# Kernel tuning notes

Measured on AMD Instinct MI355X. Metric: run time of the kernel, lower is better.

The kernel has to match this reference:

```python
import jax, jax.numpy as jnp
import numpy as np
from jax import lax

DN = ('NCDHW', 'OIDHW', 'NCDHW')


def _ln(x, w, b, eps=1e-5):
    m = jnp.mean(x, -1, keepdims=True)
    v = jnp.mean((x - m) ** 2, -1, keepdims=True)
    return (x - m) * lax.rsqrt(v + eps) * w + b


def _gelu(x):
    return jax.nn.gelu(x, approximate=False)


def _dwconv3(v, w, b, groups):
    # depthwise 3x3x3, padding=1, stride=1; v:[B,C,H,W,D], w:[C,1,3,3,3]
    y = lax.conv_general_dilated(v, w, (1, 1, 1), 'SAME',
                                 dimension_numbers=DN,
                                 feature_group_count=groups)
    return y + b[None, :, None, None, None]


def _forward(x, ln1_w, ln1_b, q_w, sr1_w, sr1_b, n1_w, n1_b, sr2_w, sr2_b,
             n2_w, n2_b, kv1_w, kv2_w, lc1_w, lc1_b, lc2_w, lc2_b,
             proj_w, proj_b, ln2_w, ln2_b, fc1_w, fc1_b, fc2_w, fc2_b,
             H, W, D):
    B, N, C = x.shape
    h = 8
    h2 = h // 2
    hd = C // h
    scale = hd ** -0.5
    C2 = C // 2

    # ---- pre-norm + attention ----
    xa = _ln(x, ln1_w, ln1_b)
    q = (xa @ q_w.T).reshape(B, N, h, hd).transpose(0, 2, 1, 3)  # [B,h,N,hd]

    x_ = xa.transpose(0, 2, 1).reshape(B, C, H, W, D)
    # branch 1: conv k=2 s=2 spatial reduction
    y1 = lax.conv_general_dilated(x_, sr1_w, (2, 2, 2), 'VALID',
                                  dimension_numbers=DN) + sr1_b[None, :, None, None, None]
    N1 = (H // 2) * (W // 2) * (D // 2)
    x1 = _gelu(_ln(y1.reshape(B, C, N1).transpose(0, 2, 1), n1_w, n1_b))  # [B,N1,C]
    # branch 2: 1x1x1 conv, full resolution
    y2 = lax.conv_general_dilated(x_, sr2_w, (1, 1, 1), 'VALID',
                                  dimension_numbers=DN) + sr2_b[None, :, None, None, None]
    N2 = N
    x2 = _gelu(_ln(y2.reshape(B, C, N2).transpose(0, 2, 1), n2_w, n2_b))  # [B,N2,C]

    kv1 = (x1 @ kv1_w.T).reshape(B, N1, 2, h2, hd).transpose(2, 0, 3, 1, 4)
    k1, v1 = kv1[0], kv1[1]  # [B,h2,N1,hd]
    kv2 = (x2 @ kv2_w.T).reshape(B, N2, 2, h2, hd).transpose(2, 0, 3, 1, 4)
    k2, v2 = kv2[0], kv2[1]  # [B,h2,N2,hd]

    attn1 = jax.nn.softmax(jnp.einsum('bhnd,bhmd->bhnm', q[:, :h2], k1) * scale, axis=-1)
    v1sp = v1.transpose(0, 2, 1, 3).reshape(B, N1, C2).transpose(0, 2, 1).reshape(
        B, C2, H // 2, W // 2, D // 2)
    v1 = v1 + _dwconv3(v1sp, lc1_w, lc1_b, C2).reshape(B, h2, hd, N1).transpose(0, 1, 3, 2)
    o1 = jnp.einsum('bhnm,bhmd->bhnd', attn1, v1).transpose(0, 2, 1, 3).reshape(B, N, C2)

    attn2 = jax.nn.softmax(jnp.einsum('bhnd,bhmd->bhnm', q[:, h2:], k2) * scale, axis=-1)
    v2sp = v2.transpose(0, 2, 1, 3).reshape(B, N2, C2).transpose(0, 2, 1).reshape(B, C2, H, W, D)
    v2 = v2 + _dwconv3(v2sp, lc2_w, lc2_b, C2).reshape(B, h2, hd, N2).transpose(0, 1, 3, 2)
    o2 = jnp.einsum('bhnm,bhmd->bhnd', attn2, v2).transpose(0, 2, 1, 3).reshape(B, N, C2)

    att = jnp.concatenate([o1, o2], axis=-1) @ proj_w.T + proj_b
    x = x + att  # residual (drop_path = 0)

    # ---- pre-norm + MLP ----
    xm = _ln(x, ln2_w, ln2_b)
    mlp = _gelu(xm @ fc1_w.T + fc1_b) @ fc2_w.T + fc2_b
    return x + mlp


def setup_inputs() -> dict:
    key = jax.random.key(0)
    B, C, H, W, D = 2, 384, 16, 16, 16
    N = H * W * D
    hid = 4 * C
    C2 = C // 2
    ks = iter(jax.random.split(key, 32))
    rn = lambda shape, s=0.02: (jax.random.normal(next(ks), shape) * s).astype(jnp.float32)
    return {
        'x': jax.random.normal(next(ks), (B, N, C), jnp.float32),
        'ln1_w': jnp.ones(C, jnp.float32), 'ln1_b': jnp.zeros(C, jnp.float32),
        'q_w': rn((C, C)),
        'sr1_w': rn((C, C, 2, 2, 2), 0.025), 'sr1_b': jnp.zeros(C, jnp.float32),
        'n1_w': jnp.ones(C, jnp.float32), 'n1_b': jnp.zeros(C, jnp.float32),
        'sr2_w': rn((C, C, 1, 1, 1), 0.07), 'sr2_b': jnp.zeros(C, jnp.float32),
        'n2_w': jnp.ones(C, jnp.float32), 'n2_b': jnp.zeros(C, jnp.float32),
        'kv1_w': rn((C, C)), 'kv2_w': rn((C, C)),
        'lc1_w': rn((C2, 1, 3, 3, 3), 0.27), 'lc1_b': jnp.zeros(C2, jnp.float32),
        'lc2_w': rn((C2, 1, 3, 3, 3), 0.27), 'lc2_b': jnp.zeros(C2, jnp.float32),
        'proj_w': rn((C, C)), 'proj_b': jnp.zeros(C, jnp.float32),
        'ln2_w': jnp.ones(C, jnp.float32), 'ln2_b': jnp.zeros(C, jnp.float32),
        'fc1_w': rn((hid, C)), 'fc1_b': jnp.zeros(hid, jnp.float32),
        'fc2_w': rn((C, hid)), 'fc2_b': jnp.zeros(C, jnp.float32),
        'H': H, 'W': W, 'D': D,
    }


def reference(x, ln1_w, ln1_b, q_w, sr1_w, sr1_b, n1_w, n1_b, sr2_w, sr2_b,
              n2_w, n2_b, kv1_w, kv2_w, lc1_w, lc1_b, lc2_w, lc2_b,
              proj_w, proj_b, ln2_w, ln2_b, fc1_w, fc1_b, fc2_w, fc2_b,
              H, W, D):
    return _forward(x, ln1_w, ln1_b, q_w, sr1_w, sr1_b, n1_w, n1_b, sr2_w, sr2_b,
                    n2_w, n2_b, kv1_w, kv2_w, lc1_w, lc1_b, lc2_w, lc2_b,
                    proj_w, proj_b, ln2_w, ln2_b, fc1_w, fc1_b, fc2_w, fc2_b,
                    H, W, D)
```

## Files before the change

kernel.cpp:

```cpp
#include <hip/hip_runtime.h>

typedef unsigned short ushort_t;
typedef unsigned int uint_t;
typedef __bf16 bf16_t;
typedef __bf16 bf16x8 __attribute__((ext_vector_type(8)));
typedef float f32x4 __attribute__((ext_vector_type(4)));

__device__ __forceinline__ float b2f(ushort_t u) {
    union { uint_t i; float f; } v; v.i = ((uint_t)u) << 16; return v.f;
}
__device__ __forceinline__ ushort_t f2b(float f) {
    union { float f; uint_t i; } v; v.f = f;
    uint_t r = v.i + 0x7fffu + ((v.i >> 16) & 1u);
    return (ushort_t)(r >> 16);
}
__device__ __forceinline__ float gelu_exact(float x) {
    return 0.5f * x * (1.0f + erff(x * 0.70710678118654752f));
}

__global__ void prep_weights(const float* __restrict__ q_w, const float* __restrict__ sr2_w,
                             const float* __restrict__ kv1_w, const float* __restrict__ kv2_w,
                             const float* __restrict__ proj_w, const float* __restrict__ fc1_w,
                             const float* __restrict__ fc2_w, const float* __restrict__ sr1_w,
                             ushort_t* __restrict__ dst) {
    int gid = blockIdx.x * 256 + threadIdx.x;
    int i = gid;
    if (i < 147456) { dst[gid] = f2b(q_w[i]); return; }
    i -= 147456;
    if (i < 147456) { dst[gid] = f2b(sr2_w[i]); return; }
    i -= 147456;
    if (i < 147456) { dst[gid] = f2b(kv1_w[i]); return; }
    i -= 147456;
    if (i < 147456) { dst[gid] = f2b(kv2_w[i]); return; }
    i -= 147456;
    if (i < 147456) { dst[gid] = f2b(proj_w[i]); return; }
    i -= 147456;
    if (i < 589824) { dst[gid] = f2b(fc1_w[i]); return; }
    i -= 589824;
    if (i < 589824) { dst[gid] = f2b(fc2_w[i]); return; }
    i -= 589824;
    if (i < 1179648) {
        int co = i / 3072, r = i % 3072, kk = r / 384, ci = r % 384;
        dst[gid] = f2b(sr1_w[((size_t)co * 384 + ci) * 8 + kk]);
    }
}

__global__ void im2col_kernel(const ushort_t* __restrict__ xa, ushort_t* __restrict__ A1) {
    int gid = blockIdx.x * 256 + threadIdx.x;
    if (gid >= 1024 * 3072) return;
    int m = gid / 3072, r = gid % 3072, kk = r / 384, ci = r % 384;
    int b = m >> 9, n1 = m & 511;
    int ho = n1 >> 6, wo = (n1 >> 3) & 7, dz = n1 & 7;
    int n = ((2 * ho + ((kk >> 2) & 1)) << 8) + ((2 * wo + ((kk >> 1) & 1)) << 4) + (2 * dz + (kk & 1));
    A1[gid] = xa[((size_t)b * 4096 + n) * 384 + ci];
}

__global__ __launch_bounds__(128) void ln_kernel(const float* __restrict__ in,
                                                 const float* __restrict__ w,
                                                 const float* __restrict__ b,
                                                 float* __restrict__ outf,
                                                 ushort_t* __restrict__ outb, int act) {
    const int C = 384;
    int row = blockIdx.x, tid = threadIdx.x;
    size_t base = (size_t)row * C;
    float x[3], s = 0.f, s2 = 0.f;
#pragma unroll
    for (int i = 0; i < 3; i++) {
        int c = tid + i * 128;
        float v = in[base + c];
        x[i] = v; s += v; s2 += v * v;
    }
    for (int off = 32; off; off >>= 1) { s += __shfl_down(s, off); s2 += __shfl_down(s2, off); }
    __shared__ float sc[4];
    int lane = tid & 63, wid = tid >> 6;
    if (lane == 0) { sc[wid] = s; sc[wid + 2] = s2; }
    __syncthreads();
    float ts = sc[0] + sc[1], ts2 = sc[2] + sc[3];
    float mean = ts / C;
    float var = ts2 / C - mean * mean;
    float rstd = rsqrtf(var + 1e-5f);
#pragma unroll
    for (int i = 0; i < 3; i++) {
        int c = tid + i * 128;
        float v = (x[i] - mean) * rstd * w[c] + b[c];
        if (act) v = gelu_exact(v);
        if (outf) outf[base + c] = v;
        if (outb) outb[base + c] = f2b(v);
    }
}

__global__ __launch_bounds__(256) void mfma_gemm(const ushort_t* __restrict__ A,
                                                 const ushort_t* __restrict__ W,
                                                 const float* __restrict__ bias,
                                                 const float* __restrict__ res,
                                                 float* __restrict__ outf,
                                                 ushort_t* __restrict__ outb,
                                                 int M, int N, int K, int act) {
    __shared__ bf16_t Asl[128][40];
    __shared__ bf16_t Wsl[128][40];
    int tid = threadIdx.x;
    int wave = tid >> 6, lane = tid & 63, g = lane >> 4, c = lane & 15;
    int wm = wave >> 1, wn = wave & 1;
    int m0 = blockIdx.y * 128, n0 = blockIdx.x * 128;
    int srow = tid >> 1, sseg = tid & 1;
    const ushort_t* Abase = A + (size_t)(m0 + srow) * K + sseg * 16;
    const ushort_t* Wbase = W + (size_t)(n0 + srow) * K + sseg * 16;

    f32x4 acc[4][4];
#pragma unroll
    for (int i = 0; i < 4; i++)
#pragma unroll
        for (int j = 0; j < 4; j++) acc[i][j] = f32x4{0.f, 0.f, 0.f, 0.f};

    uint4 av0 = *(const uint4*)Abase, av1 = *(const uint4*)(Abase + 8);
    uint4 wv0 = *(const uint4*)Wbase, wv1 = *(const uint4*)(Wbase + 8);
    for (int k0 = 0; k0 < K; k0 += 32) {
        __syncthreads();
        *(uint4*)&Asl[srow][sseg * 16] = av0;
        *(uint4*)&Asl[srow][sseg * 16 + 8] = av1;
        *(uint4*)&Wsl[srow][sseg * 16] = wv0;
        *(uint4*)&Wsl[srow][sseg * 16 + 8] = wv1;
        __syncthreads();
        uint4 nav0, nav1, nwv0, nwv1;
        bool more = (k0 + 32 < K);
        if (more) {
            nav0 = *(const uint4*)(Abase + k0 + 32);
            nav1 = *(const uint4*)(Abase + k0 + 40);
            nwv0 = *(const uint4*)(Wbase + k0 + 32);
            nwv1 = *(const uint4*)(Wbase + k0 + 40);
        }
        bf16x8 af[4], bf[4];
#pragma unroll
        for (int fi = 0; fi < 4; fi++) af[fi] = *(bf16x8*)&Asl[wm * 64 + fi * 16 + c][g * 8];
#pragma unroll
        for (int fj = 0; fj < 4; fj++) bf[fj] = *(bf16x8*)&Wsl[wn * 64 + fj * 16 + c][g * 8];
#pragma unroll
        for (int fi = 0; fi < 4; fi++)
#pragma unroll
            for (int fj = 0; fj < 4; fj++)
                acc[fi][fj] = __builtin_amdgcn_mfma_f32_16x16x32_bf16(af[fi], bf[fj], acc[fi][fj], 0, 0, 0);
        if (more) { av0 = nav0; av1 = nav1; wv0 = nwv0; wv1 = nwv1; }
    }

#pragma unroll
    for (int fi = 0; fi < 4; fi++) {
#pragma unroll
        for (int fj = 0; fj < 4; fj++) {
            int n = n0 + wn * 64 + fj * 16 + c;
            float bv = bias ? bias[n] : 0.f;
#pragma unroll
            for (int i = 0; i < 4; i++) {
                int m = m0 + wm * 64 + fi * 16 + 4 * g + i;
                float v = acc[fi][fj][i] + bv;
                if (act == 1) v = gelu_exact(v);
                size_t idx = (size_t)m * N + n;
                if (res) v += res[idx];
                if (outf) outf[idx] = v;
                if (outb) outb[idx] = f2b(v);
            }
        }
    }
}

__global__ __launch_bounds__(256) void gemm64(const ushort_t* __restrict__ A,
                                              const ushort_t* __restrict__ W,
                                              const float* __restrict__ bias,
                                              const float* __restrict__ res,
                                              float* __restrict__ outf,
                                              ushort_t* __restrict__ outb,
                                              int M, int N, int K, int act, float oscale) {
    __shared__ bf16_t Asl[64][72];
    __shared__ bf16_t Wsl[64][72];
    int tid = threadIdx.x;
    int wave = tid >> 6, lane = tid & 63, g = lane >> 4, c = lane & 15;
    int wm = wave >> 1, wn = wave & 1;
    int m0 = blockIdx.y * 64, n0 = blockIdx.x * 64;
    int srow = tid >> 2, sseg = tid & 3;
    const ushort_t* Abase = A + (size_t)(m0 + srow) * K + sseg * 16;
    const ushort_t* Wbase = W + (size_t)(n0 + srow) * K + sseg * 16;

    f32x4 acc[2][2];
#pragma unroll
    for (int i = 0; i < 2; i++)
#pragma unroll
        for (int j = 0; j < 2; j++) acc[i][j] = f32x4{0.f, 0.f, 0.f, 0.f};

    uint4 av0 = *(const uint4*)Abase, av1 = *(const uint4*)(Abase + 8);
    uint4 wv0 = *(const uint4*)Wbase, wv1 = *(const uint4*)(Wbase + 8);
    for (int k0 = 0; k0 < K; k0 += 64) {
        __syncthreads();
        *(uint4*)&Asl[srow][sseg * 16] = av0;
        *(uint4*)&Asl[srow][sseg * 16 + 8] = av1;
        *(uint4*)&Wsl[srow][sseg * 16] = wv0;
        *(uint4*)&Wsl[srow][sseg * 16 + 8] = wv1;
        __syncthreads();
        uint4 nav0, nav1, nwv0, nwv1;
        bool more = (k0 + 64 < K);
        if (more) {
            nav0 = *(const uint4*)(Abase + k0 + 64);
            nav1 = *(const uint4*)(Abase + k0 + 72);
            nwv0 = *(const uint4*)(Wbase + k0 + 64);
            nwv1 = *(const uint4*)(Wbase + k0 + 72);
        }
#pragma unroll
        for (int kk = 0; kk < 2; kk++) {
            bf16x8 af[2], bf[2];
#pragma unroll
            for (int fi = 0; fi < 2; fi++) af[fi] = *(bf16x8*)&Asl[wm * 32 + fi * 16 + c][kk * 32 + g * 8];
#pragma unroll
            for (int fj = 0; fj < 2; fj++) bf[fj] = *(bf16x8*)&Wsl[wn * 32 + fj * 16 + c][kk * 32 + g * 8];
#pragma unroll
            for (int fi = 0; fi < 2; fi++)
#pragma unroll
                for (int fj = 0; fj < 2; fj++)
                    acc[fi][fj] = __builtin_amdgcn_mfma_f32_16x16x32_bf16(af[fi], bf[fj], acc[fi][fj], 0, 0, 0);
        }
        if (more) { av0 = nav0; av1 = nav1; wv0 = nwv0; wv1 = nwv1; }
    }

#pragma unroll
    for (int fi = 0; fi < 2; fi++) {
#pragma unroll
        for (int fj = 0; fj < 2; fj++) {
            int n = n0 + wn * 32 + fj * 16 + c;
            float bv = bias ? bias[n] : 0.f;
#pragma unroll
            for (int i = 0; i < 4; i++) {
                int m = m0 + wm * 32 + fi * 16 + 4 * g + i;
                float v = (acc[fi][fj][i] + bv) * oscale;
                if (act == 1) v = gelu_exact(v);
                size_t idx = (size_t)m * N + n;
                if (res) v += res[idx];
                if (outf) outf[idx] = v;
                if (outb) outb[idx] = f2b(v);
            }
        }
    }
}

__global__ __launch_bounds__(256) void gemm_qy2(const ushort_t* __restrict__ A,
                                                const ushort_t* __restrict__ W,
                                                const float* __restrict__ sr2_b,
                                                ushort_t* __restrict__ qb,
                                                float* __restrict__ y2f,
                                                int M, float qscale) {
    const int K = 384;
    __shared__ bf16_t Asl[64][72];
    __shared__ bf16_t Wsl[64][72];
    int tid = threadIdx.x;
    int wave = tid >> 6, lane = tid & 63, g = lane >> 4, c = lane & 15;
    int wm = wave >> 1, wn = wave & 1;
    int m0 = blockIdx.y * 64, n0 = blockIdx.x * 64;
    int srow = tid >> 2, sseg = tid & 3;
    const ushort_t* Abase = A + (size_t)(m0 + srow) * K + sseg * 16;
    const ushort_t* Wbase = W + (size_t)(n0 + srow) * K + sseg * 16;

    f32x4 acc[2][2];
#pragma unroll
    for (int i = 0; i < 2; i++)
#pragma unroll
        for (int j = 0; j < 2; j++) acc[i][j] = f32x4{0.f, 0.f, 0.f, 0.f};

    uint4 av0 = *(const uint4*)Abase, av1 = *(const uint4*)(Abase + 8);
    uint4 wv0 = *(const uint4*)Wbase, wv1 = *(const uint4*)(Wbase + 8);
    for (int k0 = 0; k0 < K; k0 += 64) {
        __syncthreads();
        *(uint4*)&Asl[srow][sseg * 16] = av0;
        *(uint4*)&Asl[srow][sseg * 16 + 8] = av1;
        *(uint4*)&Wsl[srow][sseg * 16] = wv0;
        *(uint4*)&Wsl[srow][sseg * 16 + 8] = wv1;
        __syncthreads();
        uint4 nav0, nav1, nwv0, nwv1;
        bool more = (k0 + 64 < K);
        if (more) {
            nav0 = *(const uint4*)(Abase + k0 + 64);
            nav1 = *(const uint4*)(Abase + k0 + 72);
            nwv0 = *(const uint4*)(Wbase + k0 + 64);
            nwv1 = *(const uint4*)(Wbase + k0 + 72);
        }
#pragma unroll
        for (int kk = 0; kk < 2; kk++) {
            bf16x8 af[2], bf[2];
#pragma unroll
            for (int fi = 0; fi < 2; fi++) af[fi] = *(bf16x8*)&Asl[wm * 32 + fi * 16 + c][kk * 32 + g * 8];
#pragma unroll
            for (int fj = 0; fj < 2; fj++) bf[fj] = *(bf16x8*)&Wsl[wn * 32 + fj * 16 + c][kk * 32 + g * 8];
#pragma unroll
            for (int fi = 0; fi < 2; fi++)
#pragma unroll
                for (int fj = 0; fj < 2; fj++)
                    acc[fi][fj] = __builtin_amdgcn_mfma_f32_16x16x32_bf16(af[fi], bf[fj], acc[fi][fj], 0, 0, 0);
        }
        if (more) { av0 = nav0; av1 = nav1; wv0 = nwv0; wv1 = nwv1; }
    }

    int isq = (n0 < 384);
#pragma unroll
    for (int fi = 0; fi < 2; fi++) {
#pragma unroll
        for (int fj = 0; fj < 2; fj++) {
            int n = n0 + wn * 32 + fj * 16 + c;
#pragma unroll
            for (int i = 0; i < 4; i++) {
                int m = m0 + wm * 32 + fi * 16 + 4 * g + i;
                float v = acc[fi][fj][i];
                if (isq) {
                    qb[(size_t)m * 384 + n] = f2b(v * qscale);
                } else {
                    y2f[(size_t)m * 384 + (n - 384)] = v + sr2_b[n - 384];
                }
            }
        }
    }
}

__device__ __forceinline__ void dwconv_one(const ushort_t* __restrict__ vin,
                                           const float* __restrict__ wt,
                                           const float* __restrict__ bias,
                                           ushort_t* __restrict__ vout,
                                           int Hs, int Wsz, int Ds, int S, int gid) {
    int c2 = gid % 192;
    int r = gid / 192;
    int n = r % S;
    int b = r / S;
    int dz = n % Ds, wy = (n / Ds) % Wsz, hx = n / (Wsz * Ds);
    float center = b2f(vin[(size_t)(b * S + n) * 384 + c2]);
    float acc = bias[c2];
    for (int kh = -1; kh <= 1; kh++) {
        int h2 = hx + kh; if (h2 < 0 || h2 >= Hs) continue;
        for (int kw = -1; kw <= 1; kw++) {
            int w2 = wy + kw; if (w2 < 0 || w2 >= Wsz) continue;
            for (int kd = -1; kd <= 1; kd++) {
                int d2 = dz + kd; if (d2 < 0 || d2 >= Ds) continue;
                int nn = (h2 * Wsz + w2) * Ds + d2;
                acc += b2f(vin[(size_t)(b * S + nn) * 384 + c2]) *
                       wt[c2 * 27 + (kh + 1) * 9 + (kw + 1) * 3 + (kd + 1)];
            }
        }
    }
    vout[(size_t)(b * S + n) * 192 + c2] = f2b(center + acc);
}

__global__ void dwconv2_kernel(const ushort_t* __restrict__ v2in, const ushort_t* __restrict__ v1in,
                               const float* __restrict__ w2, const float* __restrict__ b2,
                               const float* __restrict__ w1, const float* __restrict__ b1,
                               ushort_t* __restrict__ vo2, ushort_t* __restrict__ vo1) {
    int gid = blockIdx.x * 256 + threadIdx.x;
    const int T2 = 2 * 4096 * 192;
    const int T1 = 2 * 512 * 192;
    if (gid < T2) dwconv_one(v2in, w2, b2, vo2, 16, 16, 16, 4096, gid);
    else if (gid < T2 + T1) dwconv_one(v1in, w1, b1, vo1, 8, 8, 8, 512, gid - T2);
}

__global__ __launch_bounds__(256) void transpose2_kernel(const ushort_t* __restrict__ src2,
                                                         ushort_t* __restrict__ dst2,
                                                         const ushort_t* __restrict__ src1,
                                                         ushort_t* __restrict__ dst1) {
    __shared__ ushort_t t_lds[64][65];
    int bx = blockIdx.x;
    const ushort_t* src; ushort_t* dst; int S, n0;
    if (bx < 64) { src = src2; dst = dst2; S = 4096; n0 = bx * 64; }
    else         { src = src1; dst = dst1; S = 512;  n0 = (bx - 64) * 64; }
    int c0 = blockIdx.y * 64, b = blockIdx.z;
    int tid = threadIdx.x;
#pragma unroll
    for (int i = 0; i < 16; i++) {
        int idx = tid + i * 256;
        int r = idx >> 6, cc = idx & 63;
        t_lds[r][cc] = src[((size_t)b * S + n0 + r) * 192 + c0 + cc];
    }
    __syncthreads();
#pragma unroll
    for (int i = 0; i < 16; i++) {
        int idx = tid + i * 256;
        int r = idx >> 6, cc = idx & 63;
        dst[((size_t)b * 192 + c0 + r) * S + n0 + cc] = t_lds[cc][r];
    }
}

__global__ __launch_bounds__(256, 4) void attn_mfma5s(
    const ushort_t* __restrict__ qbuf,
    const ushort_t* __restrict__ kv1,
    const ushort_t* __restrict__ kv2,
    const ushort_t* __restrict__ vt1,
    const ushort_t* __restrict__ vt2,
    ushort_t* __restrict__ obuf)
{
    __shared__ __align__(16) char lds_raw[18432];
    bf16_t (*P)[32][72] = (bf16_t (*)[32][72])lds_raw;
    float (*CF)[64][14] = (float (*)[64][14])lds_raw;

    const int N = 4096;
    int tid = threadIdx.x;
    int q0 = blockIdx.x * 32, hl = 7 - blockIdx.y, b = blockIdx.z;
    int wave = tid >> 6, lane = tid & 63, g = lane >> 4, c = lane & 15;
    int br2 = hl >> 2;
    int NK = br2 ? 4096 : 512;
    const ushort_t* kbuf = br2 ? kv2 : kv1;
    const ushort_t* vtb  = br2 ? vt2 : vt1;
    int hloc = hl & 3;
    int NKc = NK >> 2;
    int kb0 = wave * NKc;
    int nkt = NKc >> 6;

    union { uint4 u; bf16x8 v; } zz; zz.u = uint4{0u, 0u, 0u, 0u};
    const bf16x8 zero8 = zz.v;

    bf16x8 bq0[2], bq1[2];
#pragma unroll
    for (int qg = 0; qg < 2; qg++) {
        const ushort_t* qrowp = qbuf + ((size_t)b * N + q0 + qg * 16 + c) * 384 + hl * 48;
        bq0[qg] = *(const bf16x8*)(qrowp + g * 8);
        bq1[qg] = (g < 2) ? *(const bf16x8*)(qrowp + 32 + g * 8) : zero8;
    }

    f32x4 of[3][2];
#pragma unroll
    for (int dt = 0; dt < 3; dt++)
#pragma unroll
        for (int qg = 0; qg < 2; qg++) of[dt][qg] = f32x4{0.f, 0.f, 0.f, 0.f};
    float l_acc[2] = {0.f, 0.f};

    const ushort_t* kp = kbuf + ((size_t)b * NK + kb0 + c) * 384 + hloc * 48;
    const ushort_t* vp = vtb + ((size_t)b * 192 + hloc * 48 + c) * NK + kb0;

    for (int kt = 0; kt < nkt; kt++) {
        f32x4 sf[4][2];
#pragma unroll
        for (int t = 0; t < 4; t++)
#pragma unroll
            for (int qg = 0; qg < 2; qg++) sf[t][qg] = f32x4{0.f, 0.f, 0.f, 0.f};
        __builtin_amdgcn_s_setprio(1);
#pragma unroll
        for (int t = 0; t < 4; t++) {
            const ushort_t* kr = kp + (size_t)(kt * 64 + 16 * t) * 384;
            bf16x8 ak0 = *(const bf16x8*)(kr + g * 8);
            bf16x8 ak1 = (g < 2) ? *(const bf16x8*)(kr + 32 + g * 8) : zero8;
#pragma unroll
            for (int qg = 0; qg < 2; qg++) {
                sf[t][qg] = __builtin_amdgcn_mfma_f32_16x16x32_bf16(ak0, bq0[qg], sf[t][qg], 0, 0, 0);
                sf[t][qg] = __builtin_amdgcn_mfma_f32_16x16x32_bf16(ak1, bq1[qg], sf[t][qg], 0, 0, 0);
            }
        }
        __builtin_amdgcn_s_setprio(0);

#pragma unroll
        for (int qg = 0; qg < 2; qg++) {
#pragma unroll
            for (int t = 0; t < 4; t++) {
                union { ushort4 v; bf16_t h[4]; } pk;
#pragma unroll
                for (int i = 0; i < 4; i++) {
                    float p = exp2f(sf[t][qg][i]);
                    l_acc[qg] += p;
                    pk.h[i] = (bf16_t)p;
                }
                *(ushort4*)&P[wave][qg * 16 + c][16 * t + 4 * g] = pk.v;
            }
        }

        asm volatile("s_waitcnt lgkmcnt(0)" ::: "memory");

        bf16x8 pb0[2], pb1[2];
#pragma unroll
        for (int qg = 0; qg < 2; qg++) {
            pb0[qg] = *(bf16x8*)&P[wave][qg * 16 + c][g * 8];
            pb1[qg] = *(bf16x8*)&P[wave][qg * 16 + c][32 + g * 8];
        }
        __builtin_amdgcn_s_setprio(1);
#pragma unroll
        for (int dt = 0; dt < 3; dt++) {
            const ushort_t* vr = vp + (size_t)(16 * dt) * NK + kt * 64;
            bf16x8 av0 = *(const bf16x8*)(vr + g * 8);
            bf16x8 av1 = *(const bf16x8*)(vr + 32 + g * 8);
#pragma unroll
            for (int qg = 0; qg < 2; qg++) {
                of[dt][qg] = __builtin_amdgcn_mfma_f32_16x16x32_bf16(av0, pb0[qg], of[dt][qg], 0, 0, 0);
                of[dt][qg] = __builtin_amdgcn_mfma_f32_16x16x32_bf16(av1, pb1[qg], of[dt][qg], 0, 0, 0);
            }
        }
        __builtin_amdgcn_s_setprio(0);
    }

#pragma unroll
    for (int qg = 0; qg < 2; qg++) {
        l_acc[qg] += __shfl_xor(l_acc[qg], 16);
        l_acc[qg] += __shfl_xor(l_acc[qg], 32);
    }

#pragma unroll
    for (int qg = 0; qg < 2; qg++) {
        __syncthreads();
        float* cfp = &CF[wave][lane][0];
#pragma unroll
        for (int dt = 0; dt < 3; dt++)
#pragma unroll
            for (int i = 0; i < 4; i++) cfp[dt * 4 + i] = of[dt][qg][i];
        cfp[12] = l_acc[qg];
        __syncthreads();
        if (wave == 0) {
            float lsum = 0.f;
            float oc[12];
#pragma unroll
            for (int j = 0; j < 12; j++) oc[j] = 0.f;
#pragma unroll
            for (int w = 0; w < 4; w++) {
                lsum += CF[w][lane][12];
#pragma unroll
                for (int j = 0; j < 12; j++) oc[j] += CF[w][lane][j];
            }
            float rl = 1.f / lsum;
            int qrow = q0 + qg * 16 + c;
#pragma unroll
            for (int dt = 0; dt < 3; dt++) {
                union { ushort4 v; bf16_t h[4]; } pk;
#pragma unroll
                for (int i = 0; i < 4; i++) pk.h[i] = (bf16_t)(oc[dt * 4 + i] * rl);
                *(ushort4*)&obuf[((size_t)b * N + qrow) * 384 + hl * 48 + 16 * dt + 4 * g] = pk.v;
            }
        }
    }
}

extern "C" void kernel_launch(void* const* d_in, const int* in_sizes, int n_in,
                              void* d_out, int out_size, void* d_ws, size_t ws_size,
                              hipStream_t stream) {
    const int B = 2, N = 4096, C = 384, N1 = 512, HID = 1536;
    const float* x      = (const float*)d_in[0];
    const float* ln1_w  = (const float*)d_in[1];
    const float* ln1_b  = (const float*)d_in[2];
    const float* q_w    = (const float*)d_in[3];
    const float* sr1_w  = (const float*)d_in[4];
    const float* sr1_b  = (const float*)d_in[5];
    const float* n1_w   = (const float*)d_in[6];
    const float* n1_b   = (const float*)d_in[7];
    const float* sr2_w  = (const float*)d_in[8];
    const float* sr2_b  = (const float*)d_in[9];
    const float* n2_w   = (const float*)d_in[10];
    const float* n2_b   = (const float*)d_in[11];
    const float* kv1_w  = (const float*)d_in[12];
    const float* kv2_w  = (const float*)d_in[13];
    const float* lc1_w  = (const float*)d_in[14];
    const float* lc1_b  = (const float*)d_in[15];
    const float* lc2_w  = (const float*)d_in[16];
    const float* lc2_b  = (const float*)d_in[17];
    const float* proj_w = (const float*)d_in[18];
    const float* proj_b = (const float*)d_in[19];
    const float* ln2_w  = (const float*)d_in[20];
    const float* ln2_b  = (const float*)d_in[21];
    const float* fc1_w  = (const float*)d_in[22];
    const float* fc1_b  = (const float*)d_in[23];
    const float* fc2_w  = (const float*)d_in[24];
    const float* fc2_b  = (const float*)d_in[25];
    float* out = (float*)d_out;

    char* ws = (char*)d_ws;
    ushort_t* wbase = (ushort_t*)ws;
    ushort_t* wqy2 = wbase;
    ushort_t* wkv1 = wbase + 294912;
    ushort_t* wkv2 = wbase + 442368;
    ushort_t* wproj= wbase + 589824;
    ushort_t* wfc1 = wbase + 737280;
    ushort_t* wfc2 = wbase + 1327104;
    ushort_t* wsr1 = wbase + 1916928;
    ushort_t* xa_bf = (ushort_t*)(ws + 6193152);
    ushort_t* qbB   = (ushort_t*)(ws + 12484608);
    ushort_t* x2_bf = (ushort_t*)(ws + 18776064);
    ushort_t* kv2   = (ushort_t*)(ws + 25067520);
    ushort_t* vmod2 = (ushort_t*)(ws + 31358976);
    ushort_t* kv1   = (ushort_t*)(ws + 34504704);
    ushort_t* vmod1 = (ushort_t*)(ws + 35291136);
    ushort_t* x1_bf = (ushort_t*)(ws + 35684352);
    float*    y2f   = (float*)(ws + 36470784);
    float*    y1f   = (float*)(ws + 49053696);
    ushort_t* A1    = (ushort_t*)(ws + 50626560);
    ushort_t* hid   = (ushort_t*)(ws + 56918016);
    ushort_t* vt2   = (ushort_t*)(ws + 82083840);
    ushort_t* vt1   = (ushort_t*)(ws + 85229568);
    ushort_t* Obuf  = xa_bf;
    float*    xres  = y2f;
    ushort_t* xm_bf = A1;

    const float QSCALE = 0.14433756729740643f * 1.4426950408889634f;

    prep_weights<<<(3096576 + 255) / 256, 256, 0, stream>>>(q_w, sr2_w, kv1_w, kv2_w,
                                                            proj_w, fc1_w, fc2_w, sr1_w, wbase);
    ln_kernel<<<B * N, 128, 0, stream>>>(x, ln1_w, ln1_b, nullptr, xa_bf, 0);
    gemm_qy2<<<dim3(12, 128), 256, 0, stream>>>(xa_bf, wqy2, sr2_b, qbB, y2f, B * N, QSCALE);
    ln_kernel<<<B * N, 128, 0, stream>>>(y2f, n2_w, n2_b, nullptr, x2_bf, 1);
    im2col_kernel<<<(1024 * 3072 + 255) / 256, 256, 0, stream>>>(xa_bf, A1);
    gemm64<<<dim3(6, 16), 256, 0, stream>>>(A1, wsr1, sr1_b, nullptr,
                                            y1f, nullptr, 1024, C, 3072, 0, 1.f);
    ln_kernel<<<B * N1, 128, 0, stream>>>(y1f, n1_w, n1_b, nullptr, x1_bf, 1);
    gemm64<<<dim3(6, 128), 256, 0, stream>>>(x2_bf, wkv2, nullptr, nullptr,
                                             nullptr, kv2, B * N, C, C, 0, 1.f);
    gemm64<<<dim3(6, 16), 256, 0, stream>>>(x1_bf, wkv1, nullptr, nullptr,
                                            nullptr, kv1, 1024, C, C, 0, 1.f);
    {
        const int T2 = B * N * 192, T1 = B * N1 * 192;
        dwconv2_kernel<<<(T2 + T1 + 255) / 256, 256, 0, stream>>>(kv2 + 192, kv1 + 192,
                                                                  lc2_w, lc2_b, lc1_w, lc1_b,
                                                                  vmod2, vmod1);
        transpose2_kernel<<<dim3(72, 3, 2), 256, 0, stream>>>(vmod2, vt2, vmod1, vt1);
    }
    attn_mfma5s<<<dim3(N / 32, 8, B), 256, 0, stream>>>(qbB, kv1, kv2, vt1, vt2, Obuf);
    gemm64<<<dim3(6, 128), 256, 0, stream>>>(Obuf, wproj, proj_b, x,
                                             xres, nullptr, B * N, C, C, 0, 1.f);
    ln_kernel<<<B * N, 128, 0, stream>>>(xres, ln2_w, ln2_b, nullptr, xm_bf, 0);
    mfma_gemm<<<dim3(12, 64), 256, 0, stream>>>(xm_bf, wfc1, fc1_b, nullptr,
                                                nullptr, hid, B * N, HID, C, 1);
    gemm64<<<dim3(6, 128), 256, 0, stream>>>(hid, wfc2, fc2_b, xres,
                                             out, nullptr, B * N, C, HID, 0, 1.f);
}
```

Baseline: 334.1 us.

## Split-K the strided sr1 conv GEMM and merge the two KV GEMMs into one launch

The K=3072 sr1 GEMM on only 1024 rows previously ran as 96 blocks. It now uses a 4-way split-K over 384 blocks that write fp32 partials, and a new LayerNorm kernel sums the partials, adds the conv bias, then applies LN and GELU. The kv1 and kv2 projection GEMMs are fused into a single launch that picks the operand set from blockIdx.y. This targets GPU underutilization and launch overhead, at the cost of extra partial-sum memory traffic and a larger workspace.

Result: faster. 313.6 us (-6.1%).

```diff
diff --git a/kernel.cpp b/kernel.cpp
--- a/kernel.cpp
+++ b/kernel.cpp
@@ -89,6 +89,40 @@
     }
 }
 
+__global__ __launch_bounds__(128) void ln4_kernel(const float* __restrict__ p,
+                                                  const float* __restrict__ cbias,
+                                                  const float* __restrict__ w,
+                                                  const float* __restrict__ b,
+                                                  ushort_t* __restrict__ outb) {
+    const int C = 384;
+    const size_t CH = (size_t)1024 * 384;
+    int row = blockIdx.x, tid = threadIdx.x;
+    size_t base = (size_t)row * C;
+    float x[3], s = 0.f, s2 = 0.f;
+#pragma unroll
+    for (int i = 0; i < 3; i++) {
+        int c = tid + i * 128;
+        float v = ((p[base + c] + p[CH + base + c]) + (p[2 * CH + base + c] + p[3 * CH + base + c]))
+                  + cbias[c];
+        x[i] = v; s += v; s2 += v * v;
+    }
+    for (int off = 32; off; off >>= 1) { s += __shfl_down(s, off); s2 += __shfl_down(s2, off); }
+    __shared__ float sc[4];
+    int lane = tid & 63, wid = tid >> 6;
+    if (lane == 0) { sc[wid] = s; sc[wid + 2] = s2; }
+    __syncthreads();
+    float ts = sc[0] + sc[1], ts2 = sc[2] + sc[3];
+    float mean = ts / C;
+    float var = ts2 / C - mean * mean;
+    float rstd = rsqrtf(var + 1e-5f);
+#pragma unroll
+    for (int i = 0; i < 3; i++) {
+        int c = tid + i * 128;
+        float v = (x[i] - mean) * rstd * w[c] + b[c];
+        outb[base + c] = f2b(gelu_exact(v));
+    }
+}
+
 __global__ __launch_bounds__(256) void mfma_gemm(const ushort_t* __restrict__ A,
                                                  const ushort_t* __restrict__ W,
                                                  const float* __restrict__ bias,
@@ -233,6 +267,149 @@
                 if (res) v += res[idx];
                 if (outf) outf[idx] = v;
                 if (outb) outb[idx] = f2b(v);
+            }
+        }
+    }
+}
+
+__global__ __launch_bounds__(256) void gemm64sk(const ushort_t* __restrict__ A,
+                                                const ushort_t* __restrict__ W,
+                                                float* __restrict__ yp) {
+    const int K = 3072, N = 384, KC = 768;
+    __shared__ bf16_t Asl[64][72];
+    __shared__ bf16_t Wsl[64][72];
+    int tid = threadIdx.x;
+    int wave = tid >> 6, lane = tid & 63, g = lane >> 4, c = lane & 15;
+    int wm = wave >> 1, wn = wave & 1;
+    int m0 = blockIdx.y * 64, n0 = blockIdx.x * 64, kc = blockIdx.z;
+    int kbeg = kc * KC;
+    int srow = tid >> 2, sseg = tid & 3;
+    const ushort_t* Abase = A + (size_t)(m0 + srow) * K + kbeg + sseg * 16;
+    const ushort_t* Wbase = W + (size_t)(n0 + srow) * K + kbeg + sseg * 16;
+    float* out = yp + (size_t)kc * 1024 * 384;
+
+    f32x4 acc[2][2];
+#pragma unroll
+    for (int i = 0; i < 2; i++)
+#pragma unroll
+        for (int j = 0; j < 2; j++) acc[i][j] = f32x4{0.f, 0.f, 0.f, 0.f};
+
+    uint4 av0 = *(const uint4*)Abase, av1 = *(const uint4*)(Abase + 8);
+    uint4 wv0 = *(const uint4*)Wbase, wv1 = *(const uint4*)(Wbase + 8);
+    for (int k0 = 0; k0 < KC; k0 += 64) {
+        __syncthreads();
+        *(uint4*)&Asl[srow][sseg * 16] = av0;
+        *(uint4*)&Asl[srow][sseg * 16 + 8] = av1;
+        *(uint4*)&Wsl[srow][sseg * 16] = wv0;
+        *(uint4*)&Wsl[srow][sseg * 16 + 8] = wv1;
+        __syncthreads();
+        uint4 nav0, nav1, nwv0, nwv1;
+        bool more = (k0 + 64 < KC);
+        if (more) {
+            nav0 = *(const uint4*)(Abase + k0 + 64);
+            nav1 = *(const uint4*)(Abase + k0 + 72);
+            nwv0 = *(const uint4*)(Wbase + k0 + 64);
+            nwv1 = *(const uint4*)(Wbase + k0 + 72);
+        }
+#pragma unroll
+        for (int kk = 0; kk < 2; kk++) {
+            bf16x8 af[2], bf[2];
+#pragma unroll
+            for (int fi = 0; fi < 2; fi++) af[fi] = *(bf16x8*)&Asl[wm * 32 + fi * 16 + c][kk * 32 + g * 8];
+#pragma unroll
+            for (int fj = 0; fj < 2; fj++) bf[fj] = *(bf16x8*)&Wsl[wn * 32 + fj * 16 + c][kk * 32 + g * 8];
+#pragma unroll
+            for (int fi = 0; fi < 2; fi++)
+#pragma unroll
+                for (int fj = 0; fj < 2; fj++)
+                    acc[fi][fj] = __builtin_amdgcn_mfma_f32_16x16x32_bf16(af[fi], bf[fj], acc[fi][fj], 0, 0, 0);
+        }
+        if (more) { av0 = nav0; av1 = nav1; wv0 = nwv0; wv1 = nwv1; }
+    }
+
+#pragma unroll
+    for (int fi = 0; fi < 2; fi++) {
+#pragma unroll
+        for (int fj = 0; fj < 2; fj++) {
+            int n = n0 + wn * 32 + fj * 16 + c;
+#pragma unroll
+            for (int i = 0; i < 4; i++) {
+                int m = m0 + wm * 32 + fi * 16 + 4 * g + i;
+                out[(size_t)m * N + n] = acc[fi][fj][i];
+            }
+        }
+    }
+}
+
+__global__ __launch_bounds__(256) void gemm_kv(const ushort_t* __restrict__ A2,
+                                               const ushort_t* __restrict__ W2,
+                                               ushort_t* __restrict__ O2,
+                                               const ushort_t* __restrict__ A1,
+                                               const ushort_t* __restrict__ W1,
+                                               ushort_t* __restrict__ O1) {
+    const int K = 384, N = 384;
+    __shared__ bf16_t Asl[64][72];
+    __shared__ bf16_t Wsl[64][72];
+    int tid = threadIdx.x;
+    int wave = tid >> 6, lane = tid & 63, g = lane >> 4, c = lane & 15;
+    int wm = wave >> 1, wn = wave & 1;
+    int by = blockIdx.y;
+    const ushort_t* A; const ushort_t* W; ushort_t* O; int m0;
+    if (by < 128) { A = A2; W = W2; O = O2; m0 = by * 64; }
+    else          { A = A1; W = W1; O = O1; m0 = (by - 128) * 64; }
+    int n0 = blockIdx.x * 64;
+    int srow = tid >> 2, sseg = tid & 3;
+    const ushort_t* Abase = A + (size_t)(m0 + srow) * K + sseg * 16;
+    const ushort_t* Wbase = W + (size_t)(n0 + srow) * K + sseg * 16;
+
+    f32x4 acc[2][2];
+#pragma unroll
+    for (int i = 0; i < 2; i++)
+#pragma unroll
+        for (int j = 0; j < 2; j++) acc[i][j] = f32x4{0.f, 0.f, 0.f, 0.f};
+
+    uint4 av0 = *(const uint4*)Abase, av1 = *(const uint4*)(Abase + 8);
+    uint4 wv0 = *(const uint4*)Wbase, wv1 = *(const uint4*)(Wbase + 8);
+    for (int k0 = 0; k0 < K; k0 += 64) {
+        __syncthreads();
+        *(uint4*)&Asl[srow][sseg * 16] = av0;
+        *(uint4*)&Asl[srow][sseg * 16 + 8] = av1;
+        *(uint4*)&Wsl[srow][sseg * 16] = wv0;
+        *(uint4*)&Wsl[srow][sseg * 16 + 8] = wv1;
+        __syncthreads();
+        uint4 nav0, nav1, nwv0, nwv1;
+        bool more = (k0 + 64 < K);
+        if (more) {
+            nav0 = *(const uint4*)(Abase + k0 + 64);
+            nav1 = *(const uint4*)(Abase + k0 + 72);
+            nwv0 = *(const uint4*)(Wbase + k0 + 64);
+            nwv1 = *(const uint4*)(Wbase + k0 + 72);
+        }
+#pragma unroll
+        for (int kk = 0; kk < 2; kk++) {
+            bf16x8 af[2], bf[2];
+#pragma unroll
+            for (int fi = 0; fi < 2; fi++) af[fi] = *(bf16x8*)&Asl[wm * 32 + fi * 16 + c][kk * 32 + g * 8];
+#pragma unroll
+            for (int fj = 0; fj < 2; fj++) bf[fj] = *(bf16x8*)&Wsl[wn * 32 + fj * 16 + c][kk * 32 + g * 8];
+#pragma unroll
+            for (int fi = 0; fi < 2; fi++)
+#pragma unroll
+                for (int fj = 0; fj < 2; fj++)
+                    acc[fi][fj] = __builtin_amdgcn_mfma_f32_16x16x32_bf16(af[fi], bf[fj], acc[fi][fj], 0, 0, 0);
+        }
+        if (more) { av0 = nav0; av1 = nav1; wv0 = nwv0; wv1 = nwv1; }
+    }
+
+#pragma unroll
+    for (int fi = 0; fi < 2; fi++) {
+#pragma unroll
+        for (int fj = 0; fj < 2; fj++) {
+            int n = n0 + wn * 32 + fj * 16 + c;
+#pragma unroll
+            for (int i = 0; i < 4; i++) {
+                int m = m0 + wm * 32 + fi * 16 + 4 * g + i;
+                O[(size_t)m * N + n] = f2b(acc[fi][fj][i]);
             }
         }
     }
@@ -577,9 +754,11 @@
     ushort_t* hid   = (ushort_t*)(ws + 56918016);
     ushort_t* vt2   = (ushort_t*)(ws + 82083840);
     ushort_t* vt1   = (ushort_t*)(ws + 85229568);
+    float*    y1p   = (float*)(ws + 85622784);
     ushort_t* Obuf  = xa_bf;
     float*    xres  = y2f;
     ushort_t* xm_bf = A1;
+    (void)y1f;
 
     const float QSCALE = 0.14433756729740643f * 1.4426950408889634f;
 
@@ -589,13 +768,9 @@
     gemm_qy2<<<dim3(12, 128), 256, 0, stream>>>(xa_bf, wqy2, sr2_b, qbB, y2f, B * N, QSCALE);
     ln_kernel<<<B * N, 128, 0, stream>>>(y2f, n2_w, n2_b, nullptr, x2_bf, 1);
     im2col_kernel<<<(1024 * 3072 + 255) / 256, 256, 0, stream>>>(xa_bf, A1);
-    gemm64<<<dim3(6, 16), 256, 0, stream>>>(A1, wsr1, sr1_b, nullptr,
-                                            y1f, nullptr, 1024, C, 3072, 0, 1.f);
-    ln_kernel<<<B * N1, 128, 0, stream>>>(y1f, n1_w, n1_b, nullptr, x1_bf, 1);
-    gemm64<<<dim3(6, 128), 256, 0, stream>>>(x2_bf, wkv2, nullptr, nullptr,
-                                             nullptr, kv2, B * N, C, C, 0, 1.f);
-    gemm64<<<dim3(6, 16), 256, 0, stream>>>(x1_bf, wkv1, nullptr, nullptr,
-                                            nullptr, kv1, 1024, C, C, 0, 1.f);
+    gemm64sk<<<dim3(6, 16, 4), 256, 0, stream>>>(A1, wsr1, y1p);
+    ln4_kernel<<<B * N1, 128, 0, stream>>>(y1p, sr1_b, n1_w, n1_b, x1_bf);
+    gemm_kv<<<dim3(6, 144), 256, 0, stream>>>(x2_bf, wkv2, kv2, x1_bf, wkv1, kv1);
     {
         const int T2 = B * N * 192, T1 = B * N1 * 192;
         dwconv2_kernel<<<(T2 + T1 + 255) / 256, 256, 0, stream>>>(kv2 + 192, kv1 + 192,
```
